# Kernel tuning notes

Hardware: AMD Instinct MI355X
Metric: run time of the kernel (lower is better)

Reference implementation:

```python
import jax, jax.numpy as jnp
import numpy as np

B, S, D_IN, D_OUT = 4, 4096, 1024, 64

def setup_inputs() -> dict:
    key = jax.random.key(0)
    ks = jax.random.split(key, 7)
    return {
        "x":  jax.random.normal(ks[0], (B, S, D_IN), dtype=jnp.float32),
        "Wq": jax.random.normal(ks[1], (D_IN, D_OUT), dtype=jnp.float32) * 0.02,
        "bq": jax.random.normal(ks[2], (D_OUT,), dtype=jnp.float32) * 0.02,
        "Wk": jax.random.normal(ks[3], (D_IN, D_OUT), dtype=jnp.float32) * 0.02,
        "bk": jax.random.normal(ks[4], (D_OUT,), dtype=jnp.float32) * 0.02,
        "Wv": jax.random.normal(ks[5], (D_IN, D_OUT), dtype=jnp.float32) * 0.02,
        "bv": jax.random.normal(ks[6], (D_OUT,), dtype=jnp.float32) * 0.02,
    }

def reference(x, Wq, bq, Wk, bk, Wv, bv):
    # x: [B, S, d_in]
    seq = x.shape[1]
    q = x @ Wq + bq            # [B, S, d_out]
    k = x @ Wk + bk
    v = x @ Wv + bv
    scores = jnp.einsum("bqd,bkd->bqk", q, k)          # [B, S, S]
    causal = jnp.triu(jnp.ones((seq, seq), dtype=bool), k=1)
    scores = jnp.where(causal[None, :, :], -jnp.inf, scores)
    # NOTE: original code scales by sqrt(token_len), not sqrt(d_out) (d_k = keys.shape[1])
    scale = jnp.sqrt(jnp.asarray(seq, dtype=scores.dtype))
    attn = jax.nn.softmax(scores / scale, axis=-1)      # [B, S, S]
    # dropout in the original is applied but its result is discarded -> no-op
    return jnp.einsum("bqk,bkd->bqd", attn, v)          # [B, S, d_out]
```

## Files before the change

### kernel.cpp

```cpp
#include <hip/hip_runtime.h>
#include <math.h>

#define B 4
#define S 4096
#define DIN 1024
#define DOUT 64
#define BS (B * S)

typedef __bf16 bf16;
typedef __bf16 bf16x4 __attribute__((ext_vector_type(4)));
typedef __bf16 bf16x8 __attribute__((ext_vector_type(8)));
typedef float f32x4 __attribute__((ext_vector_type(4)));

#define QSCALE 0.022542110013890053f

#define QS_OFF 0
#define K_OFF  (2u * 1024 * 1024)
#define VT_OFF (4u * 1024 * 1024)
#define WP_OFF (6u * 1024 * 1024)
#define OP_OFF (7u * 1024 * 1024)
#define LP_OFF (15u * 1024 * 1024)

__global__ __launch_bounds__(256) void wpack_kernel(
    const float* __restrict__ Wq, const float* __restrict__ Wk,
    const float* __restrict__ Wv, bf16* __restrict__ wp) {
  const int t = blockIdx.x * 256 + threadIdx.x;
  const int m = t >> 16;
  const int r = t & 65535;
  const int k = r >> 6;
  const int n64 = r & 63;
  const float* W = (m == 0) ? Wq : (m == 1) ? Wk : Wv;
  const float v = W[r];
  const int n = m * 64 + n64;
  const int nt = n >> 4;
  const int lane = ((k >> 3) & 3) * 16 + (n & 15);
  const int idx = ((nt * 32 + (k >> 5)) * 64 + lane) * 8 + (k & 7);
  wp[idx] = (bf16)v;
}

__global__ __launch_bounds__(256) void qkv_mfma_kernel(
    const float* __restrict__ x, const float* __restrict__ bq,
    const float* __restrict__ bk, const float* __restrict__ bv,
    const bf16* __restrict__ wp, bf16* __restrict__ Qs,
    bf16* __restrict__ Kb, bf16* __restrict__ VT) {
  __shared__ __align__(16) bf16 xt[2][32][40];

  const int tid = threadIdx.x;
  const int wid = tid >> 6;
  const int lane = tid & 63;
  const int l15 = lane & 15;
  const int quad = lane >> 4;
  const int blk = blockIdx.x;

  const int srow = tid >> 3;
  const int scol = (tid & 7) * 4;
  const float* xs = x + (size_t)(blk * 32 + srow) * DIN + scol;
  const bf16x8* wp8 = (const bf16x8*)wp;

  f32x4 acc[3][2];
#pragma unroll
  for (int j = 0; j < 3; ++j)
#pragma unroll
    for (int st = 0; st < 2; ++st) acc[j][st] = (f32x4)(0.f);

  {
    const float4 r0 = *(const float4*)(xs);
    bf16x4 c;
    c[0] = (bf16)r0.x; c[1] = (bf16)r0.y; c[2] = (bf16)r0.z; c[3] = (bf16)r0.w;
    *(bf16x4*)&xt[0][srow][scol] = c;
  }
  float4 rn = *(const float4*)(xs + 32);
  __syncthreads();

  for (int kc = 0; kc < 32; ++kc) {
    const int buf = kc & 1;

    bf16x8 bfr[3];
#pragma unroll
    for (int j = 0; j < 3; ++j)
      bfr[j] = wp8[((wid * 3 + j) * 32 + kc) * 64 + lane];

    const bf16x8 a0 = *(const bf16x8*)&xt[buf][l15][quad * 8];
    const bf16x8 a1 = *(const bf16x8*)&xt[buf][16 + l15][quad * 8];

#pragma unroll
    for (int j = 0; j < 3; ++j) {
      acc[j][0] = __builtin_amdgcn_mfma_f32_16x16x32_bf16(a0, bfr[j], acc[j][0], 0, 0, 0);
      acc[j][1] = __builtin_amdgcn_mfma_f32_16x16x32_bf16(a1, bfr[j], acc[j][1], 0, 0, 0);
    }

    if (kc + 1 < 32) {
      bf16x4 c;
      c[0] = (bf16)rn.x; c[1] = (bf16)rn.y; c[2] = (bf16)rn.z; c[3] = (bf16)rn.w;
      *(bf16x4*)&xt[buf ^ 1][srow][scol] = c;
      if (kc + 2 < 32) rn = *(const float4*)(xs + (kc + 2) * 32);
    }
    __syncthreads();
  }

#pragma unroll
  for (int j = 0; j < 3; ++j) {
    const int nt = wid * 3 + j;
    const int sel = nt >> 2;
    const int c = (nt & 3) * 16 + l15;
    const float* bb = (sel == 0) ? bq : (sel == 1) ? bk : bv;
    const float bias = bb[c];
#pragma unroll
    for (int st = 0; st < 2; ++st) {
      const int row0 = blk * 32 + st * 16 + quad * 4;
      if (sel == 2) {
        const int b = row0 >> 12;
        const int s0 = row0 & 4095;
        bf16x4 vv;
#pragma unroll
        for (int r = 0; r < 4; ++r) vv[r] = (bf16)(acc[j][st][r] + bias);
        *(bf16x4*)(VT + ((size_t)b * DOUT + c) * S + s0) = vv;
      } else {
        const float scale = (sel == 0) ? QSCALE : 1.f;
        bf16* ob = (sel == 0) ? Qs : Kb;
#pragma unroll
        for (int r = 0; r < 4; ++r)
          ob[(size_t)(row0 + r) * DOUT + c] = (bf16)((acc[j][st][r] + bias) * scale);
      }
    }
  }
}

__global__ __launch_bounds__(256, 4) void attn_mfma_kernel(
    const bf16* __restrict__ Qs, const bf16* __restrict__ Kb,
    const bf16* __restrict__ VT, bf16* __restrict__ Oh,
    float* __restrict__ lh) {
  __shared__ __align__(16) bf16 kt[64][72];
  __shared__ __align__(16) bf16 vt[64][72];
  __shared__ __align__(16) bf16 pw[4][16][72];

  const int tid = threadIdx.x;
  const int wid = tid >> 6;
  const int lane = tid & 63;
  const int l15 = lane & 15;
  const int quad = lane >> 4;
  const int b = blockIdx.x & 3;
  const int quarter = (blockIdx.x >> 2) & 3;
  const int strip = 63 - (blockIdx.x >> 4);
  const int ntiles = strip + 1;
  const int t0 = (quarter * ntiles) >> 2;
  const int t1 = ((quarter + 1) * ntiles) >> 2;

  const bf16* Qb = Qs + ((size_t)b * S + strip * 64 + wid * 16) * DOUT;
  const bf16* Kbase = Kb + (size_t)b * S * DOUT;
  const bf16* VTb = VT + (size_t)b * DOUT * S;

  const bf16x8 qf0 = *(const bf16x8*)(Qb + l15 * DOUT + quad * 8);
  const bf16x8 qf1 = *(const bf16x8*)(Qb + l15 * DOUT + 32 + quad * 8);

  const int c0 = tid * 2, c1 = tid * 2 + 1;
  const int r0 = c0 >> 3, q0 = (c0 & 7) * 8;
  const int r1 = c1 >> 3, q1 = (c1 & 7) * 8;

  f32x4 o[4];
#pragma unroll
  for (int i = 0; i < 4; ++i) o[i] = (f32x4)(0.f);
  f32x4 lsum = (f32x4)(0.f);

  bf16x8 kg0, kg1, vg0, vg1;
  if (t0 < t1) {
    const bf16* Kt = Kbase + (size_t)t0 * 64 * DOUT;
    kg0 = *(const bf16x8*)(Kt + r0 * DOUT + q0);
    kg1 = *(const bf16x8*)(Kt + r1 * DOUT + q1);
    vg0 = *(const bf16x8*)(VTb + (size_t)r0 * S + t0 * 64 + q0);
    vg1 = *(const bf16x8*)(VTb + (size_t)r1 * S + t0 * 64 + q1);
  }

  for (int t = t0; t < t1; ++t) {
    __syncthreads();
    *(bf16x8*)&kt[r0][q0] = kg0;
    *(bf16x8*)&kt[r1][q1] = kg1;
    *(bf16x8*)&vt[r0][q0] = vg0;
    *(bf16x8*)&vt[r1][q1] = vg1;
    if (t + 1 < t1) {
      const bf16* Kt = Kbase + (size_t)(t + 1) * 64 * DOUT;
      kg0 = *(const bf16x8*)(Kt + r0 * DOUT + q0);
      kg1 = *(const bf16x8*)(Kt + r1 * DOUT + q1);
      vg0 = *(const bf16x8*)(VTb + (size_t)r0 * S + (t + 1) * 64 + q0);
      vg1 = *(const bf16x8*)(VTb + (size_t)r1 * S + (t + 1) * 64 + q1);
    }
    __syncthreads();

    bf16x8 kf[8];
#pragma unroll
    for (int nt = 0; nt < 4; ++nt)
#pragma unroll
      for (int c = 0; c < 2; ++c)
        kf[nt * 2 + c] = *(const bf16x8*)&kt[nt * 16 + l15][c * 32 + quad * 8];

    f32x4 s[4];
#pragma unroll
    for (int nt = 0; nt < 4; ++nt) {
      s[nt] = __builtin_amdgcn_mfma_f32_16x16x32_bf16(qf0, kf[nt * 2 + 0],
                                                      (f32x4)(0.f), 0, 0, 0);
      s[nt] = __builtin_amdgcn_mfma_f32_16x16x32_bf16(qf1, kf[nt * 2 + 1],
                                                      s[nt], 0, 0, 0);
    }

    if (t == ntiles - 1) {
#pragma unroll
      for (int nt = 0; nt < 4; ++nt) {
        const int key = t * 64 + nt * 16 + l15;
#pragma unroll
        for (int r = 0; r < 4; ++r) {
          const int qrow = strip * 64 + wid * 16 + quad * 4 + r;
          const float p = (key <= qrow) ? exp2f(fminf(s[nt][r], 44.f)) : 0.f;
          lsum[r] += p;
          pw[wid][quad * 4 + r][nt * 16 + l15] = (bf16)p;
        }
      }
    } else {
#pragma unroll
      for (int nt = 0; nt < 4; ++nt)
#pragma unroll
        for (int r = 0; r < 4; ++r) {
          const float p = exp2f(fminf(s[nt][r], 44.f));
          lsum[r] += p;
          pw[wid][quad * 4 + r][nt * 16 + l15] = (bf16)p;
        }
    }

    const bf16x8 pf0 = *(const bf16x8*)&pw[wid][l15][quad * 8];
    const bf16x8 pf1 = *(const bf16x8*)&pw[wid][l15][32 + quad * 8];

#pragma unroll
    for (int ntd = 0; ntd < 4; ++ntd) {
      const bf16x8 vf0 = *(const bf16x8*)&vt[ntd * 16 + l15][quad * 8];
      const bf16x8 vf1 = *(const bf16x8*)&vt[ntd * 16 + l15][32 + quad * 8];
      o[ntd] = __builtin_amdgcn_mfma_f32_16x16x32_bf16(pf0, vf0, o[ntd], 0, 0, 0);
      o[ntd] = __builtin_amdgcn_mfma_f32_16x16x32_bf16(pf1, vf1, o[ntd], 0, 0, 0);
    }
  }

#pragma unroll
  for (int m = 1; m < 16; m <<= 1)
#pragma unroll
    for (int r = 0; r < 4; ++r) lsum[r] += __shfl_xor(lsum[r], m, 64);

  const int slot = (b * 64 + strip) * 4 + quarter;
  if (l15 == 0) {
#pragma unroll
    for (int r = 0; r < 4; ++r)
      lh[slot * 64 + wid * 16 + quad * 4 + r] = lsum[r];
  }
#pragma unroll
  for (int ntd = 0; ntd < 4; ++ntd)
#pragma unroll
    for (int r = 0; r < 4; ++r)
      Oh[(size_t)slot * 4096 + (wid * 16 + quad * 4 + r) * 64 + ntd * 16 + l15] =
          (bf16)o[ntd][r];
}

__global__ __launch_bounds__(256) void combine_kernel(
    const bf16* __restrict__ Oh, const float* __restrict__ lh,
    float* __restrict__ out) {
  const int gid = blockIdx.x * 256 + threadIdx.x;
  const int token = gid >> 4;
  const int d4 = (gid & 15) * 4;
  const int bq = token >> 12;
  const int s = token & 4095;
  const int strip = s >> 6;
  const int qq = s & 63;
  const int slot0 = (bq * 64 + strip) * 4;
  f32x4 acc = (f32x4)(0.f);
  float l = 0.f;
#pragma unroll
  for (int q = 0; q < 4; ++q) {
    const bf16x4 ov =
        *(const bf16x4*)(Oh + (size_t)(slot0 + q) * 4096 + qq * 64 + d4);
#pragma unroll
    for (int i = 0; i < 4; ++i) acc[i] += (float)ov[i];
    l += lh[(slot0 + q) * 64 + qq];
  }
  ((f32x4*)out)[gid] = acc * (1.f / l);
}

extern "C" void kernel_launch(void* const* d_in, const int* in_sizes, int n_in,
                              void* d_out, int out_size, void* d_ws,
                              size_t ws_size, hipStream_t stream) {
  const float* x  = (const float*)d_in[0];
  const float* Wq = (const float*)d_in[1];
  const float* bq = (const float*)d_in[2];
  const float* Wk = (const float*)d_in[3];
  const float* bk = (const float*)d_in[4];
  const float* Wv = (const float*)d_in[5];
  const float* bv = (const float*)d_in[6];
  float* out = (float*)d_out;

  char* ws = (char*)d_ws;
  bf16* Qs = (bf16*)(ws + QS_OFF);
  bf16* Kb = (bf16*)(ws + K_OFF);
  bf16* VT = (bf16*)(ws + VT_OFF);
  bf16* wp = (bf16*)(ws + WP_OFF);
  bf16* Oh = (bf16*)(ws + OP_OFF);
  float* lh = (float*)(ws + LP_OFF);

  wpack_kernel<<<768, 256, 0, stream>>>(Wq, Wk, Wv, wp);
  qkv_mfma_kernel<<<512, 256, 0, stream>>>(x, bq, bk, bv, wp, Qs, Kb, VT);
  attn_mfma_kernel<<<1024, 256, 0, stream>>>(Qs, Kb, VT, Oh, lh);
  combine_kernel<<<1024, 256, 0, stream>>>(Oh, lh, out);
}
```

Before: 148.2 us.

## Prepack K/V in MFMA fragment layout and split attention per-wave without LDS staging

The QKV projection now writes K and V directly in MFMA fragment order, so each attention wave can load its operands straight from global memory. This removes the shared-memory staging and the block-wide barriers in the attention loop. The attention grid now uses 32-row query strips, and the key tiles are split across 8 waves (2 blocks of 4). Each wave works independently on its own tile range, which doubles the partial outputs the combine kernel has to sum. The projection also stages x in two large 512-column phases in place of double-buffered 32-column chunks. The trade-off is more global load traffic per wave with less latency hiding, plus larger partial-result buffers.

```diff
diff --git a/kernel.cpp b/kernel.cpp
--- a/kernel.cpp
+++ b/kernel.cpp
@@ -15,11 +15,11 @@
 #define QSCALE 0.022542110013890053f
 
 #define QS_OFF 0
-#define K_OFF  (2u * 1024 * 1024)
-#define VT_OFF (4u * 1024 * 1024)
+#define KF_OFF (2u * 1024 * 1024)
+#define VF_OFF (4u * 1024 * 1024)
 #define WP_OFF (6u * 1024 * 1024)
 #define OP_OFF (7u * 1024 * 1024)
-#define LP_OFF (15u * 1024 * 1024)
+#define LP_OFF (23u * 1024 * 1024)
 
 __global__ __launch_bounds__(256) void wpack_kernel(
     const float* __restrict__ Wq, const float* __restrict__ Wk,
@@ -42,8 +42,8 @@
     const float* __restrict__ x, const float* __restrict__ bq,
     const float* __restrict__ bk, const float* __restrict__ bv,
     const bf16* __restrict__ wp, bf16* __restrict__ Qs,
-    bf16* __restrict__ Kb, bf16* __restrict__ VT) {
-  __shared__ __align__(16) bf16 xt[2][32][40];
+    bf16* __restrict__ KF, bf16* __restrict__ VF) {
+  __shared__ __align__(16) bf16 xt[32][520];
 
   const int tid = threadIdx.x;
   const int wid = tid >> 6;
@@ -52,9 +52,6 @@
   const int quad = lane >> 4;
   const int blk = blockIdx.x;
 
-  const int srow = tid >> 3;
-  const int scol = (tid & 7) * 4;
-  const float* xs = x + (size_t)(blk * 32 + srow) * DIN + scol;
   const bf16x8* wp8 = (const bf16x8*)wp;
 
   f32x4 acc[3][2];
@@ -63,39 +60,45 @@
 #pragma unroll
     for (int st = 0; st < 2; ++st) acc[j][st] = (f32x4)(0.f);
 
-  {
-    const float4 r0 = *(const float4*)(xs);
-    bf16x4 c;
-    c[0] = (bf16)r0.x; c[1] = (bf16)r0.y; c[2] = (bf16)r0.z; c[3] = (bf16)r0.w;
-    *(bf16x4*)&xt[0][srow][scol] = c;
-  }
-  float4 rn = *(const float4*)(xs + 32);
-  __syncthreads();
-
-  for (int kc = 0; kc < 32; ++kc) {
-    const int buf = kc & 1;
-
-    bf16x8 bfr[3];
-#pragma unroll
-    for (int j = 0; j < 3; ++j)
-      bfr[j] = wp8[((wid * 3 + j) * 32 + kc) * 64 + lane];
-
-    const bf16x8 a0 = *(const bf16x8*)&xt[buf][l15][quad * 8];
-    const bf16x8 a1 = *(const bf16x8*)&xt[buf][16 + l15][quad * 8];
-
-#pragma unroll
-    for (int j = 0; j < 3; ++j) {
-      acc[j][0] = __builtin_amdgcn_mfma_f32_16x16x32_bf16(a0, bfr[j], acc[j][0], 0, 0, 0);
-      acc[j][1] = __builtin_amdgcn_mfma_f32_16x16x32_bf16(a1, bfr[j], acc[j][1], 0, 0, 0);
-    }
-
-    if (kc + 1 < 32) {
-      bf16x4 c;
-      c[0] = (bf16)rn.x; c[1] = (bf16)rn.y; c[2] = (bf16)rn.z; c[3] = (bf16)rn.w;
-      *(bf16x4*)&xt[buf ^ 1][srow][scol] = c;
-      if (kc + 2 < 32) rn = *(const float4*)(xs + (kc + 2) * 32);
+  for (int ph = 0; ph < 2; ++ph) {
+    if (ph) __syncthreads();
+    {
+      float4 v[16];
+#pragma unroll
+      for (int i = 0; i < 16; ++i) {
+        const int ch = i * 256 + tid;
+        const int row = ch >> 7;
+        const int col4 = ch & 127;
+        v[i] = *(const float4*)(x + (size_t)(blk * 32 + row) * DIN + ph * 512 +
+                                col4 * 4);
+      }
+#pragma unroll
+      for (int i = 0; i < 16; ++i) {
+        const int ch = i * 256 + tid;
+        const int row = ch >> 7;
+        const int col4 = ch & 127;
+        bf16x4 c;
+        c[0] = (bf16)v[i].x; c[1] = (bf16)v[i].y;
+        c[2] = (bf16)v[i].z; c[3] = (bf16)v[i].w;
+        *(bf16x4*)&xt[row][col4 * 4] = c;
+      }
     }
     __syncthreads();
+
+#pragma unroll 4
+    for (int kc = 0; kc < 16; ++kc) {
+      bf16x8 bfr[3];
+#pragma unroll
+      for (int j = 0; j < 3; ++j)
+        bfr[j] = wp8[((wid * 3 + j) * 32 + ph * 16 + kc) * 64 + lane];
+      const bf16x8 a0 = *(const bf16x8*)&xt[l15][quad * 8 + kc * 32];
+      const bf16x8 a1 = *(const bf16x8*)&xt[16 + l15][quad * 8 + kc * 32];
+#pragma unroll
+      for (int j = 0; j < 3; ++j) {
+        acc[j][0] = __builtin_amdgcn_mfma_f32_16x16x32_bf16(a0, bfr[j], acc[j][0], 0, 0, 0);
+        acc[j][1] = __builtin_amdgcn_mfma_f32_16x16x32_bf16(a1, bfr[j], acc[j][1], 0, 0, 0);
+      }
+    }
   }
 
 #pragma unroll
@@ -103,36 +106,40 @@
     const int nt = wid * 3 + j;
     const int sel = nt >> 2;
     const int c = (nt & 3) * 16 + l15;
-    const float* bb = (sel == 0) ? bq : (sel == 1) ? bk : bv;
-    const float bias = bb[c];
+    const float bias = ((sel == 0) ? bq : (sel == 1) ? bk : bv)[c];
 #pragma unroll
     for (int st = 0; st < 2; ++st) {
       const int row0 = blk * 32 + st * 16 + quad * 4;
-      if (sel == 2) {
-        const int b = row0 >> 12;
-        const int s0 = row0 & 4095;
+      if (sel == 0) {
+#pragma unroll
+        for (int r = 0; r < 4; ++r)
+          Qs[(size_t)(row0 + r) * DOUT + c] =
+              (bf16)((acc[j][st][r] + bias) * QSCALE);
+      } else if (sel == 1) {
+        const size_t kb =
+            ((size_t)(((row0 >> 6) * 4 + ((row0 >> 4) & 3)) * 2 + (c >> 5)) * 64 +
+             ((c >> 3) & 3) * 16 + quad * 4) * 8 + (c & 7);
+#pragma unroll
+        for (int r = 0; r < 4; ++r)
+          KF[kb + r * 8] = (bf16)(acc[j][st][r] + bias);
+      } else {
+        const size_t vb =
+            ((size_t)(((row0 >> 6) * 2 + ((row0 >> 5) & 1)) * 4 + (c >> 4)) * 64 +
+             (c & 15) + 16 * ((row0 >> 3) & 3)) * 8 + (row0 & 7);
         bf16x4 vv;
 #pragma unroll
         for (int r = 0; r < 4; ++r) vv[r] = (bf16)(acc[j][st][r] + bias);
-        *(bf16x4*)(VT + ((size_t)b * DOUT + c) * S + s0) = vv;
-      } else {
-        const float scale = (sel == 0) ? QSCALE : 1.f;
-        bf16* ob = (sel == 0) ? Qs : Kb;
-#pragma unroll
-        for (int r = 0; r < 4; ++r)
-          ob[(size_t)(row0 + r) * DOUT + c] = (bf16)((acc[j][st][r] + bias) * scale);
-      }
-    }
-  }
-}
-
-__global__ __launch_bounds__(256, 4) void attn_mfma_kernel(
-    const bf16* __restrict__ Qs, const bf16* __restrict__ Kb,
-    const bf16* __restrict__ VT, bf16* __restrict__ Oh,
+        *(bf16x4*)(VF + vb) = vv;
+      }
+    }
+  }
+}
+
+__global__ __launch_bounds__(256) void attn_mfma_kernel(
+    const bf16* __restrict__ Qs, const bf16* __restrict__ KFp,
+    const bf16* __restrict__ VFp, bf16* __restrict__ Oh,
     float* __restrict__ lh) {
-  __shared__ __align__(16) bf16 kt[64][72];
-  __shared__ __align__(16) bf16 vt[64][72];
-  __shared__ __align__(16) bf16 pw[4][16][72];
+  __shared__ __align__(16) bf16 pw[4][32][72];
 
   const int tid = threadIdx.x;
   const int wid = tid >> 6;
@@ -140,120 +147,122 @@
   const int l15 = lane & 15;
   const int quad = lane >> 4;
   const int b = blockIdx.x & 3;
-  const int quarter = (blockIdx.x >> 2) & 3;
-  const int strip = 63 - (blockIdx.x >> 4);
-  const int ntiles = strip + 1;
-  const int t0 = (quarter * ntiles) >> 2;
-  const int t1 = ((quarter + 1) * ntiles) >> 2;
-
-  const bf16* Qb = Qs + ((size_t)b * S + strip * 64 + wid * 16) * DOUT;
-  const bf16* Kbase = Kb + (size_t)b * S * DOUT;
-  const bf16* VTb = VT + (size_t)b * DOUT * S;
-
-  const bf16x8 qf0 = *(const bf16x8*)(Qb + l15 * DOUT + quad * 8);
-  const bf16x8 qf1 = *(const bf16x8*)(Qb + l15 * DOUT + 32 + quad * 8);
-
-  const int c0 = tid * 2, c1 = tid * 2 + 1;
-  const int r0 = c0 >> 3, q0 = (c0 & 7) * 8;
-  const int r1 = c1 >> 3, q1 = (c1 & 7) * 8;
-
-  f32x4 o[4];
-#pragma unroll
-  for (int i = 0; i < 4; ++i) o[i] = (f32x4)(0.f);
-  f32x4 lsum = (f32x4)(0.f);
-
-  bf16x8 kg0, kg1, vg0, vg1;
-  if (t0 < t1) {
-    const bf16* Kt = Kbase + (size_t)t0 * 64 * DOUT;
-    kg0 = *(const bf16x8*)(Kt + r0 * DOUT + q0);
-    kg1 = *(const bf16x8*)(Kt + r1 * DOUT + q1);
-    vg0 = *(const bf16x8*)(VTb + (size_t)r0 * S + t0 * 64 + q0);
-    vg1 = *(const bf16x8*)(VTb + (size_t)r1 * S + t0 * 64 + q1);
-  }
+  const int half = (blockIdx.x >> 2) & 1;
+  const int s32 = 127 - (blockIdx.x >> 3);
+  const int ntiles = (s32 >> 1) + 1;
+  const int e = half * 4 + wid;
+  const int t0 = (e * ntiles) >> 3;
+  const int t1 = ((e + 1) * ntiles) >> 3;
+
+  const bf16x8* KF8 = (const bf16x8*)KFp;
+  const bf16x8* VF8 = (const bf16x8*)VFp;
+  const int tb0 = b * 64;
+
+  const bf16* Qb = Qs + ((size_t)b * S + s32 * 32) * DOUT;
+  bf16x8 qf[2][2];
+#pragma unroll
+  for (int st = 0; st < 2; ++st)
+#pragma unroll
+    for (int k = 0; k < 2; ++k)
+      qf[st][k] =
+          *(const bf16x8*)(Qb + (st * 16 + l15) * DOUT + k * 32 + quad * 8);
+
+  f32x4 o[2][4];
+#pragma unroll
+  for (int st = 0; st < 2; ++st)
+#pragma unroll
+    for (int i = 0; i < 4; ++i) o[st][i] = (f32x4)(0.f);
+  f32x4 lsum[2] = {(f32x4)(0.f), (f32x4)(0.f)};
 
   for (int t = t0; t < t1; ++t) {
-    __syncthreads();
-    *(bf16x8*)&kt[r0][q0] = kg0;
-    *(bf16x8*)&kt[r1][q1] = kg1;
-    *(bf16x8*)&vt[r0][q0] = vg0;
-    *(bf16x8*)&vt[r1][q1] = vg1;
-    if (t + 1 < t1) {
-      const bf16* Kt = Kbase + (size_t)(t + 1) * 64 * DOUT;
-      kg0 = *(const bf16x8*)(Kt + r0 * DOUT + q0);
-      kg1 = *(const bf16x8*)(Kt + r1 * DOUT + q1);
-      vg0 = *(const bf16x8*)(VTb + (size_t)r0 * S + (t + 1) * 64 + q0);
-      vg1 = *(const bf16x8*)(VTb + (size_t)r1 * S + (t + 1) * 64 + q1);
-    }
-    __syncthreads();
-
-    bf16x8 kf[8];
+    const int tb = tb0 + t;
+    bf16x8 kf[8], vf[8];
 #pragma unroll
     for (int nt = 0; nt < 4; ++nt)
 #pragma unroll
       for (int c = 0; c < 2; ++c)
-        kf[nt * 2 + c] = *(const bf16x8*)&kt[nt * 16 + l15][c * 32 + quad * 8];
-
-    f32x4 s[4];
-#pragma unroll
-    for (int nt = 0; nt < 4; ++nt) {
-      s[nt] = __builtin_amdgcn_mfma_f32_16x16x32_bf16(qf0, kf[nt * 2 + 0],
-                                                      (f32x4)(0.f), 0, 0, 0);
-      s[nt] = __builtin_amdgcn_mfma_f32_16x16x32_bf16(qf1, kf[nt * 2 + 1],
-                                                      s[nt], 0, 0, 0);
-    }
+        kf[nt * 2 + c] = KF8[(size_t)((tb * 4 + nt) * 2 + c) * 64 + lane];
+#pragma unroll
+    for (int c = 0; c < 2; ++c)
+#pragma unroll
+      for (int ntd = 0; ntd < 4; ++ntd)
+        vf[c * 4 + ntd] = VF8[(size_t)((tb * 2 + c) * 4 + ntd) * 64 + lane];
+
+    f32x4 s[2][4];
+#pragma unroll
+    for (int st = 0; st < 2; ++st)
+#pragma unroll
+      for (int nt = 0; nt < 4; ++nt) {
+        s[st][nt] = __builtin_amdgcn_mfma_f32_16x16x32_bf16(
+            qf[st][0], kf[nt * 2 + 0], (f32x4)(0.f), 0, 0, 0);
+        s[st][nt] = __builtin_amdgcn_mfma_f32_16x16x32_bf16(
+            qf[st][1], kf[nt * 2 + 1], s[st][nt], 0, 0, 0);
+      }
 
     if (t == ntiles - 1) {
 #pragma unroll
-      for (int nt = 0; nt < 4; ++nt) {
-        const int key = t * 64 + nt * 16 + l15;
-#pragma unroll
-        for (int r = 0; r < 4; ++r) {
-          const int qrow = strip * 64 + wid * 16 + quad * 4 + r;
-          const float p = (key <= qrow) ? exp2f(fminf(s[nt][r], 44.f)) : 0.f;
-          lsum[r] += p;
-          pw[wid][quad * 4 + r][nt * 16 + l15] = (bf16)p;
+      for (int st = 0; st < 2; ++st)
+#pragma unroll
+        for (int nt = 0; nt < 4; ++nt) {
+          const int key = t * 64 + nt * 16 + l15;
+#pragma unroll
+          for (int r = 0; r < 4; ++r) {
+            const int qrow = s32 * 32 + st * 16 + quad * 4 + r;
+            const float p = (key <= qrow) ? exp2f(fminf(s[st][nt][r], 44.f)) : 0.f;
+            lsum[st][r] += p;
+            pw[wid][st * 16 + quad * 4 + r][nt * 16 + l15] = (bf16)p;
+          }
         }
-      }
     } else {
 #pragma unroll
-      for (int nt = 0; nt < 4; ++nt)
-#pragma unroll
-        for (int r = 0; r < 4; ++r) {
-          const float p = exp2f(fminf(s[nt][r], 44.f));
-          lsum[r] += p;
-          pw[wid][quad * 4 + r][nt * 16 + l15] = (bf16)p;
-        }
-    }
-
-    const bf16x8 pf0 = *(const bf16x8*)&pw[wid][l15][quad * 8];
-    const bf16x8 pf1 = *(const bf16x8*)&pw[wid][l15][32 + quad * 8];
-
-#pragma unroll
-    for (int ntd = 0; ntd < 4; ++ntd) {
-      const bf16x8 vf0 = *(const bf16x8*)&vt[ntd * 16 + l15][quad * 8];
-      const bf16x8 vf1 = *(const bf16x8*)&vt[ntd * 16 + l15][32 + quad * 8];
-      o[ntd] = __builtin_amdgcn_mfma_f32_16x16x32_bf16(pf0, vf0, o[ntd], 0, 0, 0);
-      o[ntd] = __builtin_amdgcn_mfma_f32_16x16x32_bf16(pf1, vf1, o[ntd], 0, 0, 0);
+      for (int st = 0; st < 2; ++st)
+#pragma unroll
+        for (int nt = 0; nt < 4; ++nt)
+#pragma unroll
+          for (int r = 0; r < 4; ++r) {
+            const float p = exp2f(fminf(s[st][nt][r], 44.f));
+            lsum[st][r] += p;
+            pw[wid][st * 16 + quad * 4 + r][nt * 16 + l15] = (bf16)p;
+          }
+    }
+
+#pragma unroll
+    for (int st = 0; st < 2; ++st) {
+      const bf16x8 pf0 = *(const bf16x8*)&pw[wid][st * 16 + l15][quad * 8];
+      const bf16x8 pf1 = *(const bf16x8*)&pw[wid][st * 16 + l15][32 + quad * 8];
+#pragma unroll
+      for (int ntd = 0; ntd < 4; ++ntd) {
+        o[st][ntd] = __builtin_amdgcn_mfma_f32_16x16x32_bf16(
+            pf0, vf[0 * 4 + ntd], o[st][ntd], 0, 0, 0);
+        o[st][ntd] = __builtin_amdgcn_mfma_f32_16x16x32_bf16(
+            pf1, vf[1 * 4 + ntd], o[st][ntd], 0, 0, 0);
+      }
     }
   }
 
 #pragma unroll
   for (int m = 1; m < 16; m <<= 1)
 #pragma unroll
-    for (int r = 0; r < 4; ++r) lsum[r] += __shfl_xor(lsum[r], m, 64);
-
-  const int slot = (b * 64 + strip) * 4 + quarter;
+    for (int st = 0; st < 2; ++st)
+#pragma unroll
+      for (int r = 0; r < 4; ++r) lsum[st][r] += __shfl_xor(lsum[st][r], m, 64);
+
+  const int slot = (b * 128 + s32) * 8 + e;
   if (l15 == 0) {
 #pragma unroll
-    for (int r = 0; r < 4; ++r)
-      lh[slot * 64 + wid * 16 + quad * 4 + r] = lsum[r];
-  }
-#pragma unroll
-  for (int ntd = 0; ntd < 4; ++ntd)
-#pragma unroll
-    for (int r = 0; r < 4; ++r)
-      Oh[(size_t)slot * 4096 + (wid * 16 + quad * 4 + r) * 64 + ntd * 16 + l15] =
-          (bf16)o[ntd][r];
+    for (int st = 0; st < 2; ++st)
+#pragma unroll
+      for (int r = 0; r < 4; ++r)
+        lh[slot * 32 + st * 16 + quad * 4 + r] = lsum[st][r];
+  }
+#pragma unroll
+  for (int st = 0; st < 2; ++st)
+#pragma unroll
+    for (int ntd = 0; ntd < 4; ++ntd)
+#pragma unroll
+      for (int r = 0; r < 4; ++r)
+        Oh[(size_t)slot * 2048 + (st * 16 + quad * 4 + r) * 64 + ntd * 16 + l15] =
+            (bf16)o[st][ntd][r];
 }
 
 __global__ __launch_bounds__(256) void combine_kernel(
@@ -262,20 +271,20 @@
   const int gid = blockIdx.x * 256 + threadIdx.x;
   const int token = gid >> 4;
   const int d4 = (gid & 15) * 4;
-  const int bq = token >> 12;
+  const int b = token >> 12;
   const int s = token & 4095;
-  const int strip = s >> 6;
-  const int qq = s & 63;
-  const int slot0 = (bq * 64 + strip) * 4;
+  const int s32 = s >> 5;
+  const int qq = s & 31;
+  const int slot0 = (b * 128 + s32) * 8;
   f32x4 acc = (f32x4)(0.f);
   float l = 0.f;
 #pragma unroll
-  for (int q = 0; q < 4; ++q) {
+  for (int q = 0; q < 8; ++q) {
     const bf16x4 ov =
-        *(const bf16x4*)(Oh + (size_t)(slot0 + q) * 4096 + qq * 64 + d4);
+        *(const bf16x4*)(Oh + (size_t)(slot0 + q) * 2048 + qq * 64 + d4);
 #pragma unroll
     for (int i = 0; i < 4; ++i) acc[i] += (float)ov[i];
-    l += lh[(slot0 + q) * 64 + qq];
+    l += lh[(slot0 + q) * 32 + qq];
   }
   ((f32x4*)out)[gid] = acc * (1.f / l);
 }
@@ -294,14 +303,14 @@
 
   char* ws = (char*)d_ws;
   bf16* Qs = (bf16*)(ws + QS_OFF);
-  bf16* Kb = (bf16*)(ws + K_OFF);
-  bf16* VT = (bf16*)(ws + VT_OFF);
+  bf16* KF = (bf16*)(ws + KF_OFF);
+  bf16* VF = (bf16*)(ws + VF_OFF);
   bf16* wp = (bf16*)(ws + WP_OFF);
   bf16* Oh = (bf16*)(ws + OP_OFF);
   float* lh = (float*)(ws + LP_OFF);
 
   wpack_kernel<<<768, 256, 0, stream>>>(Wq, Wk, Wv, wp);
-  qkv_mfma_kernel<<<512, 256, 0, stream>>>(x, bq, bk, bv, wp, Qs, Kb, VT);
-  attn_mfma_kernel<<<1024, 256, 0, stream>>>(Qs, Kb, VT, Oh, lh);
+  qkv_mfma_kernel<<<512, 256, 0, stream>>>(x, bq, bk, bv, wp, Qs, KF, VF);
+  attn_mfma_kernel<<<1024, 256, 0, stream>>>(Qs, KF, VF, Oh, lh);
   combine_kernel<<<1024, 256, 0, stream>>>(Oh, lh, out);
 }
```

Result: no change. 148.1 us (-0.0%).
